# Optimization experiments

Measured on AMD Instinct MI355X. Metric: run time of the kernel, lower is better.

## Reference

```python
import jax, jax.numpy as jnp
import numpy as np

NUM_HEADS = 8
NUM_KV_HEADS = 2
HEAD_DIM = 64
EPS = 1e-6
ROPE_BASE = 10000.0


def rmsnorm(x, w):
    # x: (..., head_dim)
    var = jnp.mean(x * x, axis=-1, keepdims=True)
    return x * jax.lax.rsqrt(var + EPS) * w


def apply_rope(x):
    # x: (B, L, nH, hd); positions along L, standard rotate-half RoPE
    B, L, nH, hd = x.shape
    inv_freq = 1.0 / (ROPE_BASE ** (jnp.arange(0, hd, 2, dtype=jnp.float32) / hd))  # (hd/2,)
    ang = jnp.arange(L, dtype=jnp.float32)[:, None] * inv_freq[None, :]  # (L, hd/2)
    cos = jnp.concatenate([jnp.cos(ang), jnp.cos(ang)], axis=-1)[None, :, None, :]  # (1,L,1,hd)
    sin = jnp.concatenate([jnp.sin(ang), jnp.sin(ang)], axis=-1)[None, :, None, :]
    x1, x2 = jnp.split(x, 2, axis=-1)
    rot = jnp.concatenate([-x2, x1], axis=-1)
    return x * cos + rot * sin


def setup_inputs() -> dict:
    key = jax.random.key(0)
    ks = jax.random.split(key, 6)
    width = 512
    x = jax.random.normal(ks[0], (1, 16, 16, 16, width), dtype=jnp.float32)
    s = 1.0 / np.sqrt(width)
    Wq = jax.random.normal(ks[1], (width, width), dtype=jnp.float32) * s
    Wk = jax.random.normal(ks[2], (NUM_KV_HEADS * HEAD_DIM, width), dtype=jnp.float32) * s
    Wv = jax.random.normal(ks[3], (NUM_KV_HEADS * HEAD_DIM, width), dtype=jnp.float32) * s
    Wo = jax.random.normal(ks[4], (width, width), dtype=jnp.float32) * s
    q_norm_w = jnp.ones((HEAD_DIM,), dtype=jnp.float32)
    k_norm_w = jnp.ones((HEAD_DIM,), dtype=jnp.float32)
    return {"x": x, "Wq": Wq, "Wk": Wk, "Wv": Wv,
            "q_norm_w": q_norm_w, "k_norm_w": k_norm_w, "Wo": Wo}


def reference(x, Wq, Wk, Wv, q_norm_w, k_norm_w, Wo):
    B, H, W, D, C = x.shape
    L = H * W * D
    xf = x.reshape(B, L, C)
    q = (xf @ Wq.T).reshape(B, L, NUM_HEADS, HEAD_DIM)
    k = (xf @ Wk.T).reshape(B, L, NUM_KV_HEADS, HEAD_DIM)
    v = (xf @ Wv.T).reshape(B, L, NUM_KV_HEADS, HEAD_DIM)
    q = apply_rope(rmsnorm(q, q_norm_w))
    k = apply_rope(rmsnorm(k, k_norm_w))
    # (B, heads, L, hd)
    q = q.transpose(0, 2, 1, 3)
    k = k.transpose(0, 2, 1, 3)
    v = v.transpose(0, 2, 1, 3)
    repeats = NUM_HEADS // NUM_KV_HEADS
    if repeats > 1:
        k = jnp.repeat(k, repeats, axis=1)
        v = jnp.repeat(v, repeats, axis=1)
    scale = 1.0 / np.sqrt(HEAD_DIM)
    scores = jnp.einsum('bhqd,bhkd->bhqk', q, k) * scale
    attn = jax.nn.softmax(scores, axis=-1)
    out = jnp.einsum('bhqk,bhkd->bhqd', attn, v)
    out = out.transpose(0, 2, 1, 3).reshape(B, H, W, D, C)
    return out @ Wo.T
```

## Files before the change

### kernel.cpp

```cpp
#include <hip/hip_runtime.h>
#include <hip/hip_bf16.h>
#include <math.h>

#define L_SEQ 4096
#define CDIM  512
#define NH    8
#define NKV   2
#define HD    64
#define EPS   1e-6f
#define QSCALE 0.18033688011f

using short8 = __attribute__((ext_vector_type(8))) short;
using f32x4  = __attribute__((ext_vector_type(4))) float;
using f32x16 = __attribute__((ext_vector_type(16))) float;
typedef unsigned short ushort_t;

__device__ __forceinline__ ushort_t f2bf(float f) {
    union { float f; unsigned u; } c; c.f = f;
    unsigned r = c.u + 0x7FFF + ((c.u >> 16) & 1);
    return (ushort_t)(r >> 16);
}
__device__ __forceinline__ float bf2f(ushort_t u) {
    union { unsigned u; float f; } c; c.u = ((unsigned)u) << 16;
    return c.f;
}

#define GLOAD_LDS16(g, l)                                                  \
    __builtin_amdgcn_global_load_lds(                                      \
        (const __attribute__((address_space(1))) unsigned int*)(g),        \
        (__attribute__((address_space(3))) unsigned int*)(l), 16, 0, 0)

__device__ __forceinline__ short8 lds_read8(const char* p) {
    return *reinterpret_cast<const short8*>(__builtin_assume_aligned(p, 16));
}

__device__ __forceinline__ unsigned pk_bf16(float lo, float hi) {
    const __hip_bfloat162 h2 = __float22bfloat162_rn(make_float2(lo, hi));
    unsigned w; __builtin_memcpy(&w, &h2, 4);
    return w;
}

__global__ __launch_bounds__(256) void cvt_bf16(const float* __restrict__ x,
                                                const float* __restrict__ wq,
                                                const float* __restrict__ wk,
                                                const float* __restrict__ wv,
                                                const float* __restrict__ wo,
                                                ushort_t* __restrict__ xb,
                                                ushort_t* __restrict__ wqb,
                                                ushort_t* __restrict__ wkb,
                                                ushort_t* __restrict__ wvb,
                                                ushort_t* __restrict__ wob) {
    const size_t i = ((size_t)blockIdx.x * 256 + threadIdx.x) << 2;
    const float* s; ushort_t* d; size_t o;
    if (i < 2097152)      { s = x;  d = xb;  o = i; }
    else if (i < 2359296) { s = wq; d = wqb; o = i - 2097152; }
    else if (i < 2424832) { s = wk; d = wkb; o = i - 2359296; }
    else if (i < 2490368) { s = wv; d = wvb; o = i - 2424832; }
    else                  { s = wo; d = wob; o = i - 2490368; }
    const float4 v = *reinterpret_cast<const float4*>(s + o);
    ushort_t r[4] = { f2bf(v.x), f2bf(v.y), f2bf(v.z), f2bf(v.w) };
    *reinterpret_cast<uint2*>(d + o) = *reinterpret_cast<const uint2*>(r);
}

template<bool OUT_BF16>
__global__ __launch_bounds__(256) void gemm_bf16_nt(const ushort_t* __restrict__ A,
                                                    const ushort_t* __restrict__ B,
                                                    void* __restrict__ Cv,
                                                    int M, int N, int K) {
    __shared__ short As[2][4096];
    __shared__ short Bs[2][4096];

    const int tid = threadIdx.x;
    const int w = tid >> 6, lane = tid & 63;
    const int g = lane >> 4, r16 = lane & 15;
    const int wr = w >> 1, wc = w & 1;
    const int m0 = blockIdx.y * 64, n0 = blockIdx.x * 64;
    const int r7sw = (r16 & 7) << 4;

    const int lrow = lane >> 3;
    const int swzb = ((lane & 7) ^ lrow) << 4;
    const int c0 = w * 2, c1 = w * 2 + 1;
    const size_t rowK2 = (size_t)K * 2;

    const char* agA = (const char*)A + (size_t)(m0 + c0 * 8 + lrow) * rowK2 + swzb;
    const char* agB = agA + 8 * rowK2;
    const char* bgA = (const char*)B + (size_t)(n0 + c0 * 8 + lrow) * rowK2 + swzb;
    const char* bgB = bgA + 8 * rowK2;

    GLOAD_LDS16(agA, (char*)As[0] + c0 * 1024);
    GLOAD_LDS16(agB, (char*)As[0] + c1 * 1024);
    GLOAD_LDS16(bgA, (char*)Bs[0] + c0 * 1024);
    GLOAD_LDS16(bgB, (char*)Bs[0] + c1 * 1024);
    __syncthreads();

    f32x4 acc[2][2] = {};
    const int NKIT = K >> 6;
    int cur = 0;
    for (int it = 0; it < NKIT; ++it) {
        if (it + 1 < NKIT) {
            const size_t ko = (size_t)(it + 1) * 128;
            char* ad = (char*)As[cur ^ 1];
            char* bd = (char*)Bs[cur ^ 1];
            GLOAD_LDS16(agA + ko, ad + c0 * 1024);
            GLOAD_LDS16(agB + ko, ad + c1 * 1024);
            GLOAD_LDS16(bgA + ko, bd + c0 * 1024);
            GLOAD_LDS16(bgB + ko, bd + c1 * 1024);
        }
        const char* at = (const char*)As[cur];
        const char* bt = (const char*)Bs[cur];

        short8 af[2][2], bfr[2][2];
#pragma unroll
        for (int t = 0; t < 2; ++t)
#pragma unroll
            for (int ks = 0; ks < 2; ++ks) {
                af[t][ks]  = lds_read8(at + (wr * 32 + t * 16 + r16) * 128
                                          + ((ks * 64 + g * 16) ^ r7sw));
                bfr[t][ks] = lds_read8(bt + (wc * 32 + t * 16 + r16) * 128
                                          + ((ks * 64 + g * 16) ^ r7sw));
            }
        __builtin_amdgcn_s_setprio(1);
#pragma unroll
        for (int tm = 0; tm < 2; ++tm)
#pragma unroll
            for (int tn = 0; tn < 2; ++tn)
#pragma unroll
                for (int ks = 0; ks < 2; ++ks)
                    acc[tm][tn] = __builtin_amdgcn_mfma_f32_16x16x32_bf16(
                        af[tm][ks], bfr[tn][ks], acc[tm][tn], 0, 0, 0);
        __builtin_amdgcn_s_setprio(0);

        __syncthreads();
        cur ^= 1;
    }

#pragma unroll
    for (int tm = 0; tm < 2; ++tm)
#pragma unroll
        for (int tn = 0; tn < 2; ++tn)
#pragma unroll
            for (int jj = 0; jj < 4; ++jj) {
                const int row = m0 + wr * 32 + tm * 16 + g * 4 + jj;
                const int col = n0 + wc * 32 + tn * 16 + r16;
                if (OUT_BF16)
                    ((ushort_t*)Cv)[(size_t)row * N + col] = f2bf(acc[tm][tn][jj]);
                else
                    ((float*)Cv)[(size_t)row * N + col] = acc[tm][tn][jj];
            }
}

__global__ __launch_bounds__(256) void norm_rope(ushort_t* __restrict__ q,
                                                 ushort_t* __restrict__ k,
                                                 const float* __restrict__ qw,
                                                 const float* __restrict__ kw) {
    const int wid  = threadIdx.x >> 6;
    const int lane = threadIdx.x & 63;
    const long row = (long)blockIdx.x * 4 + wid;
    const long QROWS = (long)L_SEQ * NH;

    ushort_t* ptr;
    const float* w;
    int pos;
    const bool isq = (row < QROWS);
    if (isq) {
        pos = (int)(row >> 3);
        ptr = q + (size_t)pos * (NH * HD) + (int)(row & 7) * HD;
        w = qw;
    } else {
        const long r = row - QROWS;
        pos = (int)(r >> 1);
        ptr = k + (size_t)pos * (NKV * HD) + (int)(r & 1) * HD;
        w = kw;
    }

    float x = bf2f(ptr[lane]);
    float ss = x * x;
#pragma unroll
    for (int off = 32; off; off >>= 1) ss += __shfl_xor(ss, off);
    float xn = x * rsqrtf(ss * (1.0f / 64.0f) + EPS) * w[lane];

    float xp = __shfl_xor(xn, 32);
    const int i = lane & 31;
    const float inv_freq = exp2f((float)i * -0.41524101186f);
    float s, c;
    sincosf((float)pos * inv_freq, &s, &c);
    float out = (lane < 32) ? (xn * c - xp * s) : (xn * c + xp * s);
    if (isq) out *= QSCALE;
    ptr[lane] = f2bf(out);
}

__global__ __launch_bounds__(256, 4) void attn_mfma(const ushort_t* __restrict__ qb,
                                                    const ushort_t* __restrict__ kb,
                                                    const ushort_t* __restrict__ vtb,
                                                    ushort_t* __restrict__ opart,
                                                    float* __restrict__ lpart) {
    __shared__ short Ks[2][4096];
    __shared__ short Vs[2][4096];

    const int tid = threadIdx.x;
    const int w = tid >> 6, lane = tid & 63;
    const int l31 = lane & 31, hf = lane >> 5;
    const int h = blockIdx.y, hkv = h >> 2;
    const int s = blockIdx.z;
    const int kvspan = L_SEQ / gridDim.z;
    const int kvb = s * kvspan;
    const int qw = blockIdx.x * 128 + w * 32;
    const int swz = (lane & 7) << 4;

    const int lrow = lane >> 3;
    const int swzb = ((lane & 7) ^ lrow) << 4;
    const int c0 = w * 2, c1 = w * 2 + 1;

    const char* kgA = (const char*)kb + (size_t)(kvb + c0 * 8 + lrow) * (NKV * HD * 2)
                      + hkv * (HD * 2) + swzb;
    const char* kgB = kgA + 8 * (NKV * HD * 2);
    const char* vgA = (const char*)vtb + (size_t)(hkv * HD + c0 * 8 + lrow) * (L_SEQ * 2)
                      + (size_t)kvb * 2 + swzb;
    const char* vgB = vgA + 8 * (size_t)(L_SEQ * 2);

    short8 qf[4];
#pragma unroll
    for (int ks = 0; ks < 4; ++ks)
        qf[ks] = *reinterpret_cast<const short8*>(
            &qb[(size_t)(qw + l31) * CDIM + h * HD + ks * 16 + hf * 8]);

    short8 onesf;
    {
        const short ob = (l31 == 0) ? (short)0x3F80 : (short)0;
        onesf = short8{ob, ob, ob, ob, ob, ob, ob, ob};
    }

    GLOAD_LDS16(kgA, (char*)Ks[0] + c0 * 1024);
    GLOAD_LDS16(kgB, (char*)Ks[0] + c1 * 1024);
    GLOAD_LDS16(vgA, (char*)Vs[0] + c0 * 1024);
    GLOAD_LDS16(vgB, (char*)Vs[0] + c1 * 1024);
    __syncthreads();

    f32x16 oacc[2] = {};
    f32x16 oaccl = {};

    int cur = 0;
    const int nit = kvspan >> 6;
    for (int it = 0; it < nit; ++it) {
        if (it + 1 < nit) {
            const size_t ko = (size_t)(it + 1) * 64 * (NKV * HD * 2);
            const size_t vo = (size_t)(it + 1) * 128;
            char* kd = (char*)Ks[cur ^ 1];
            char* vd = (char*)Vs[cur ^ 1];
            GLOAD_LDS16(kgA + ko, kd + c0 * 1024);
            GLOAD_LDS16(kgB + ko, kd + c1 * 1024);
            GLOAD_LDS16(vgA + vo, vd + c0 * 1024);
            GLOAD_LDS16(vgB + vo, vd + c1 * 1024);
        }

        const char* kt = (const char*)Ks[cur];
        const char* vt = (const char*)Vs[cur];

        unsigned pkv[16];
#pragma unroll
        for (int sub = 0; sub < 2; ++sub) {
            f32x16 sacc = {};
            __builtin_amdgcn_s_setprio(1);
#pragma unroll
            for (int ks = 0; ks < 4; ++ks) {
                const short8 kf = lds_read8(
                    kt + (sub * 32 + l31) * 128 + ((ks * 32 + hf * 16) ^ swz));
                sacc = __builtin_amdgcn_mfma_f32_32x32x16_bf16(kf, qf[ks], sacc, 0, 0, 0);
            }
            __builtin_amdgcn_s_setprio(0);
#pragma unroll
            for (int r2 = 0; r2 < 8; ++r2)
                pkv[sub * 8 + r2] = pk_bf16(exp2f(sacc[2 * r2]), exp2f(sacc[2 * r2 + 1]));
        }

        short8 pfrag[4];
#pragma unroll
        for (int kk = 0; kk < 4; ++kk) {
            auto s0 = __builtin_amdgcn_permlane32_swap(pkv[kk * 4 + 0], pkv[kk * 4 + 2], false, false);
            auto s1 = __builtin_amdgcn_permlane32_swap(pkv[kk * 4 + 1], pkv[kk * 4 + 3], false, false);
            union { unsigned u[4]; short8 s8; } pf;
            pf.u[0] = s0[0]; pf.u[1] = s1[0]; pf.u[2] = s0[1]; pf.u[3] = s1[1];
            pfrag[kk] = pf.s8;
        }

        __builtin_amdgcn_s_setprio(1);
#pragma unroll
        for (int kk = 0; kk < 4; ++kk)
            oaccl = __builtin_amdgcn_mfma_f32_32x32x16_bf16(pfrag[kk], onesf, oaccl, 0, 0, 0);
#pragma unroll
        for (int n = 0; n < 2; ++n) {
#pragma unroll
            for (int kk = 0; kk < 4; ++kk) {
                const short8 vf = lds_read8(
                    vt + (n * 32 + l31) * 128 + ((kk * 32 + hf * 16) ^ swz));
                oacc[n] = __builtin_amdgcn_mfma_f32_32x32x16_bf16(pfrag[kk], vf, oacc[n], 0, 0, 0);
            }
        }
        __builtin_amdgcn_s_setprio(0);

        __syncthreads();
        cur ^= 1;
    }

    ushort_t* op = opart + (size_t)s * L_SEQ * CDIM;
#pragma unroll
    for (int n = 0; n < 2; ++n)
#pragma unroll
        for (int r = 0; r < 16; ++r) {
            const int row = qw + (r & 3) + 8 * (r >> 2) + 4 * hf;
            op[(size_t)row * CDIM + h * HD + n * 32 + l31] = f2bf(oacc[n][r]);
        }
    if (l31 == 0) {
        float* lp = lpart + (size_t)s * L_SEQ * NH;
#pragma unroll
        for (int r = 0; r < 16; ++r) {
            const int row = qw + (r & 3) + 8 * (r >> 2) + 4 * hf;
            lp[(size_t)row * NH + h] = oaccl[r];
        }
    }
}

__global__ __launch_bounds__(256) void combine_splits(const ushort_t* __restrict__ opart,
                                                      const float* __restrict__ lpart,
                                                      ushort_t* __restrict__ out,
                                                      int nsplit) {
    const size_t i4 = ((size_t)blockIdx.x * 256 + threadIdx.x) << 2;
    const int row = (int)(i4 >> 9);
    const int h = (int)((i4 & 511) >> 6);
    float l = 0.0f;
    for (int s = 0; s < nsplit; ++s)
        l += lpart[(size_t)s * L_SEQ * NH + (size_t)row * NH + h];
    const float inv = 1.0f / l;

    float acc[4] = {};
    for (int s = 0; s < nsplit; ++s) {
        ushort_t a[4];
        *reinterpret_cast<uint2*>(a) =
            *reinterpret_cast<const uint2*>(opart + (size_t)s * L_SEQ * CDIM + i4);
#pragma unroll
        for (int j = 0; j < 4; ++j) acc[j] += bf2f(a[j]);
    }
    ushort_t r[4];
#pragma unroll
    for (int j = 0; j < 4; ++j) r[j] = f2bf(acc[j] * inv);
    *reinterpret_cast<uint2*>(out + i4) = *reinterpret_cast<const uint2*>(r);
}

extern "C" void kernel_launch(void* const* d_in, const int* in_sizes, int n_in,
                              void* d_out, int out_size, void* d_ws, size_t ws_size,
                              hipStream_t stream) {
    const float* x   = (const float*)d_in[0];
    const float* Wq  = (const float*)d_in[1];
    const float* Wk  = (const float*)d_in[2];
    const float* Wv  = (const float*)d_in[3];
    const float* qnw = (const float*)d_in[4];
    const float* knw = (const float*)d_in[5];
    const float* Wo  = (const float*)d_in[6];
    float* out = (float*)d_out;

    const size_t tail = (size_t)L_SEQ * CDIM * 2
                      + (size_t)L_SEQ * NKV * HD * 2 * 2
                      + (size_t)CDIM * CDIM * 2 * 2
                      + (size_t)NKV * HD * CDIM * 2 * 2
                      + (size_t)8 * L_SEQ * NH * 4;
    const size_t need8 = (size_t)8 * L_SEQ * CDIM * 2 + tail;
    const int nsplit = (ws_size >= need8) ? 8 : 4;

    char* p = (char*)d_ws;
    ushort_t* opart = (ushort_t*)p;
    ushort_t* xb    = opart;
    ushort_t* abuf  = opart;
    char* q = p + (size_t)nsplit * L_SEQ * CDIM * 2;
    ushort_t* qbuf = (ushort_t*)q;
    ushort_t* kbuf = qbuf + (size_t)L_SEQ * CDIM;
    ushort_t* vtb  = kbuf + (size_t)L_SEQ * NKV * HD;
    ushort_t* wqb  = vtb  + (size_t)L_SEQ * NKV * HD;
    ushort_t* wkb  = wqb  + (size_t)CDIM * CDIM;
    ushort_t* wvb  = wkb  + (size_t)NKV * HD * CDIM;
    ushort_t* wob  = wvb  + (size_t)NKV * HD * CDIM;
    float*    lpart = (float*)(wob + (size_t)CDIM * CDIM);

    const dim3 blk(256);

    cvt_bf16<<<dim3(2688), blk, 0, stream>>>(x, Wq, Wk, Wv, Wo, xb, wqb, wkb, wvb, wob);

    gemm_bf16_nt<true><<<dim3(8, 64),  blk, 0, stream>>>(xb, wqb, qbuf, L_SEQ, CDIM, CDIM);
    gemm_bf16_nt<true><<<dim3(2, 64),  blk, 0, stream>>>(xb, wkb, kbuf, L_SEQ, NKV * HD, CDIM);
    gemm_bf16_nt<true><<<dim3(64, 2),  blk, 0, stream>>>(wvb, xb, vtb, NKV * HD, L_SEQ, CDIM);

    norm_rope<<<dim3((L_SEQ * (NH + NKV)) / 4), blk, 0, stream>>>(qbuf, kbuf, qnw, knw);

    attn_mfma<<<dim3(L_SEQ / 128, NH, nsplit), blk, 0, stream>>>(qbuf, kbuf, vtb, opart, lpart);

    combine_splits<<<dim3((L_SEQ * CDIM) / (256 * 4)), blk, 0, stream>>>(opart, lpart, abuf, nsplit);

    gemm_bf16_nt<false><<<dim3(8, 64), blk, 0, stream>>>(abuf, wob, out, L_SEQ, CDIM, CDIM);
}
```

Measured before the change: 112.3 us.

## Triple-buffer K/V loads with vmcnt waits and compute row sums in registers

Moves the attention kernel's K/V staging from double to triple buffering in LDS. It prefetches two tiles ahead and replaces the end-of-iteration __syncthreads with an explicit vmcnt wait plus barrier at the top of each iteration. It also drops the extra MFMA against a ones fragment that built the softmax denominators, accumulating the exp sums in scalar registers and reducing them across the half-wave at the end. Shared memory per block grows and the occupancy hint falls from 4 to 3 blocks. The denominator now sums the fp32 exps rather than their bf16-rounded values.

After: 111.4 us. No clear change (-0.8%).

```diff
diff --git a/kernel.cpp b/kernel.cpp
--- a/kernel.cpp
+++ b/kernel.cpp
@@ -189,13 +189,13 @@
     ptr[lane] = f2bf(out);
 }
 
-__global__ __launch_bounds__(256, 4) void attn_mfma(const ushort_t* __restrict__ qb,
+__global__ __launch_bounds__(256, 3) void attn_mfma(const ushort_t* __restrict__ qb,
                                                     const ushort_t* __restrict__ kb,
                                                     const ushort_t* __restrict__ vtb,
                                                     ushort_t* __restrict__ opart,
                                                     float* __restrict__ lpart) {
-    __shared__ short Ks[2][4096];
-    __shared__ short Vs[2][4096];
+    __shared__ short Ks[3][4096];
+    __shared__ short Vs[3][4096];
 
     const int tid = threadIdx.x;
     const int w = tid >> 6, lane = tid & 63;
@@ -224,37 +224,40 @@
         qf[ks] = *reinterpret_cast<const short8*>(
             &qb[(size_t)(qw + l31) * CDIM + h * HD + ks * 16 + hf * 8]);
 
-    short8 onesf;
     {
-        const short ob = (l31 == 0) ? (short)0x3F80 : (short)0;
-        onesf = short8{ob, ob, ob, ob, ob, ob, ob, ob};
-    }
-
-    GLOAD_LDS16(kgA, (char*)Ks[0] + c0 * 1024);
-    GLOAD_LDS16(kgB, (char*)Ks[0] + c1 * 1024);
-    GLOAD_LDS16(vgA, (char*)Vs[0] + c0 * 1024);
-    GLOAD_LDS16(vgB, (char*)Vs[0] + c1 * 1024);
-    __syncthreads();
+        GLOAD_LDS16(kgA, (char*)Ks[0] + c0 * 1024);
+        GLOAD_LDS16(kgB, (char*)Ks[0] + c1 * 1024);
+        GLOAD_LDS16(vgA, (char*)Vs[0] + c0 * 1024);
+        GLOAD_LDS16(vgB, (char*)Vs[0] + c1 * 1024);
+        const size_t ko = (size_t)64 * (NKV * HD * 2);
+        const size_t vo = 128;
+        GLOAD_LDS16(kgA + ko, (char*)Ks[1] + c0 * 1024);
+        GLOAD_LDS16(kgB + ko, (char*)Ks[1] + c1 * 1024);
+        GLOAD_LDS16(vgA + vo, (char*)Vs[1] + c0 * 1024);
+        GLOAD_LDS16(vgB + vo, (char*)Vs[1] + c1 * 1024);
+    }
 
     f32x16 oacc[2] = {};
-    f32x16 oaccl = {};
-
-    int cur = 0;
+    float lsum = 0.0f;
+
+    char* kc = (char*)Ks[0]; char* kn = (char*)Ks[1]; char* kf3 = (char*)Ks[2];
+    char* vc = (char*)Vs[0]; char* vn = (char*)Vs[1]; char* vf3 = (char*)Vs[2];
+
     const int nit = kvspan >> 6;
     for (int it = 0; it < nit; ++it) {
-        if (it + 1 < nit) {
-            const size_t ko = (size_t)(it + 1) * 64 * (NKV * HD * 2);
-            const size_t vo = (size_t)(it + 1) * 128;
-            char* kd = (char*)Ks[cur ^ 1];
-            char* vd = (char*)Vs[cur ^ 1];
-            GLOAD_LDS16(kgA + ko, kd + c0 * 1024);
-            GLOAD_LDS16(kgB + ko, kd + c1 * 1024);
-            GLOAD_LDS16(vgA + vo, vd + c0 * 1024);
-            GLOAD_LDS16(vgB + vo, vd + c1 * 1024);
-        }
-
-        const char* kt = (const char*)Ks[cur];
-        const char* vt = (const char*)Vs[cur];
+        if (it + 1 < nit) asm volatile("s_waitcnt vmcnt(4)" ::: "memory");
+        else              asm volatile("s_waitcnt vmcnt(0)" ::: "memory");
+        __builtin_amdgcn_s_barrier();
+        __builtin_amdgcn_sched_barrier(0);
+
+        if (it + 2 < nit) {
+            const size_t ko = (size_t)(it + 2) * 64 * (NKV * HD * 2);
+            const size_t vo = (size_t)(it + 2) * 128;
+            GLOAD_LDS16(kgA + ko, kf3 + c0 * 1024);
+            GLOAD_LDS16(kgB + ko, kf3 + c1 * 1024);
+            GLOAD_LDS16(vgA + vo, vf3 + c0 * 1024);
+            GLOAD_LDS16(vgB + vo, vf3 + c1 * 1024);
+        }
 
         unsigned pkv[16];
 #pragma unroll
@@ -263,14 +266,18 @@
             __builtin_amdgcn_s_setprio(1);
 #pragma unroll
             for (int ks = 0; ks < 4; ++ks) {
-                const short8 kf = lds_read8(
-                    kt + (sub * 32 + l31) * 128 + ((ks * 32 + hf * 16) ^ swz));
-                sacc = __builtin_amdgcn_mfma_f32_32x32x16_bf16(kf, qf[ks], sacc, 0, 0, 0);
+                const short8 kfr = lds_read8(
+                    kc + (sub * 32 + l31) * 128 + ((ks * 32 + hf * 16) ^ swz));
+                sacc = __builtin_amdgcn_mfma_f32_32x32x16_bf16(kfr, qf[ks], sacc, 0, 0, 0);
             }
             __builtin_amdgcn_s_setprio(0);
 #pragma unroll
-            for (int r2 = 0; r2 < 8; ++r2)
-                pkv[sub * 8 + r2] = pk_bf16(exp2f(sacc[2 * r2]), exp2f(sacc[2 * r2 + 1]));
+            for (int r2 = 0; r2 < 8; ++r2) {
+                const float x = exp2f(sacc[2 * r2]);
+                const float y = exp2f(sacc[2 * r2 + 1]);
+                lsum += x + y;
+                pkv[sub * 8 + r2] = pk_bf16(x, y);
+            }
         }
 
         short8 pfrag[4];
@@ -285,24 +292,24 @@
 
         __builtin_amdgcn_s_setprio(1);
 #pragma unroll
-        for (int kk = 0; kk < 4; ++kk)
-            oaccl = __builtin_amdgcn_mfma_f32_32x32x16_bf16(pfrag[kk], onesf, oaccl, 0, 0, 0);
-#pragma unroll
         for (int n = 0; n < 2; ++n) {
 #pragma unroll
             for (int kk = 0; kk < 4; ++kk) {
                 const short8 vf = lds_read8(
-                    vt + (n * 32 + l31) * 128 + ((kk * 32 + hf * 16) ^ swz));
+                    vc + (n * 32 + l31) * 128 + ((kk * 32 + hf * 16) ^ swz));
                 oacc[n] = __builtin_amdgcn_mfma_f32_32x32x16_bf16(pfrag[kk], vf, oacc[n], 0, 0, 0);
             }
         }
         __builtin_amdgcn_s_setprio(0);
 
-        __syncthreads();
-        cur ^= 1;
-    }
-
+        char* tk = kc; kc = kn; kn = kf3; kf3 = tk;
+        char* tv = vc; vc = vn; vn = vf3; vf3 = tv;
+    }
+
+    lsum += __shfl_xor(lsum, 32);
     ushort_t* op = opart + (size_t)s * L_SEQ * CDIM;
+    float* lp = lpart + (size_t)s * L_SEQ * NH;
+    if (lane < 32) lp[(size_t)(qw + lane) * NH + h] = lsum;
 #pragma unroll
     for (int n = 0; n < 2; ++n)
 #pragma unroll
@@ -310,14 +317,6 @@
             const int row = qw + (r & 3) + 8 * (r >> 2) + 4 * hf;
             op[(size_t)row * CDIM + h * HD + n * 32 + l31] = f2bf(oacc[n][r]);
         }
-    if (l31 == 0) {
-        float* lp = lpart + (size_t)s * L_SEQ * NH;
-#pragma unroll
-        for (int r = 0; r < 16; ++r) {
-            const int row = qw + (r & 3) + 8 * (r >> 2) + 4 * hf;
-            lp[(size_t)row * NH + h] = oaccl[r];
-        }
-    }
 }
 
 __global__ __launch_bounds__(256) void combine_splits(const ushort_t* __restrict__ opart,
```

## Double query rows per wave and compute softmax row sums with scalar adds

Applied to the files above, without the earlier changes.

Each wave now handles 64 query rows as two 32-row MFMA tiles. Every K and V fragment read from LDS is therefore reused twice, and the grid is halved. The row-sum computation moves from an extra ones-vector MFMA to per-lane float accumulation followed by a cross-half shuffle. PV accumulation is interleaved per sub-block to limit live registers. Register pressure roughly doubles, so the launch bound drops to 2 blocks per CU, which reduces occupancy and the number of blocks.

Result: slower. 115.1 us (+2.5%).

```diff
diff --git a/kernel.cpp b/kernel.cpp
--- a/kernel.cpp
+++ b/kernel.cpp
@@ -189,7 +189,7 @@
     ptr[lane] = f2bf(out);
 }
 
-__global__ __launch_bounds__(256, 4) void attn_mfma(const ushort_t* __restrict__ qb,
+__global__ __launch_bounds__(256, 2) void attn_mfma(const ushort_t* __restrict__ qb,
                                                     const ushort_t* __restrict__ kb,
                                                     const ushort_t* __restrict__ vtb,
                                                     ushort_t* __restrict__ opart,
@@ -204,7 +204,7 @@
     const int s = blockIdx.z;
     const int kvspan = L_SEQ / gridDim.z;
     const int kvb = s * kvspan;
-    const int qw = blockIdx.x * 128 + w * 32;
+    const int qw = blockIdx.x * 256 + w * 64;
     const int swz = (lane & 7) << 4;
 
     const int lrow = lane >> 3;
@@ -218,16 +218,13 @@
                       + (size_t)kvb * 2 + swzb;
     const char* vgB = vgA + 8 * (size_t)(L_SEQ * 2);
 
-    short8 qf[4];
-#pragma unroll
-    for (int ks = 0; ks < 4; ++ks)
-        qf[ks] = *reinterpret_cast<const short8*>(
+    short8 qf0[4], qf1[4];
+#pragma unroll
+    for (int ks = 0; ks < 4; ++ks) {
+        qf0[ks] = *reinterpret_cast<const short8*>(
             &qb[(size_t)(qw + l31) * CDIM + h * HD + ks * 16 + hf * 8]);
-
-    short8 onesf;
-    {
-        const short ob = (l31 == 0) ? (short)0x3F80 : (short)0;
-        onesf = short8{ob, ob, ob, ob, ob, ob, ob, ob};
+        qf1[ks] = *reinterpret_cast<const short8*>(
+            &qb[(size_t)(qw + 32 + l31) * CDIM + h * HD + ks * 16 + hf * 8]);
     }
 
     GLOAD_LDS16(kgA, (char*)Ks[0] + c0 * 1024);
@@ -236,8 +233,8 @@
     GLOAD_LDS16(vgB, (char*)Vs[0] + c1 * 1024);
     __syncthreads();
 
-    f32x16 oacc[2] = {};
-    f32x16 oaccl = {};
+    f32x16 oacc0[2] = {}, oacc1[2] = {};
+    float ls0[2] = {}, ls1[2] = {};
 
     int cur = 0;
     const int nit = kvspan >> 6;
@@ -256,68 +253,79 @@
         const char* kt = (const char*)Ks[cur];
         const char* vt = (const char*)Vs[cur];
 
-        unsigned pkv[16];
 #pragma unroll
         for (int sub = 0; sub < 2; ++sub) {
-            f32x16 sacc = {};
+            f32x16 s0 = {}, s1 = {};
             __builtin_amdgcn_s_setprio(1);
 #pragma unroll
             for (int ks = 0; ks < 4; ++ks) {
-                const short8 kf = lds_read8(
+                const short8 kfr = lds_read8(
                     kt + (sub * 32 + l31) * 128 + ((ks * 32 + hf * 16) ^ swz));
-                sacc = __builtin_amdgcn_mfma_f32_32x32x16_bf16(kf, qf[ks], sacc, 0, 0, 0);
+                s0 = __builtin_amdgcn_mfma_f32_32x32x16_bf16(kfr, qf0[ks], s0, 0, 0, 0);
+                s1 = __builtin_amdgcn_mfma_f32_32x32x16_bf16(kfr, qf1[ks], s1, 0, 0, 0);
             }
             __builtin_amdgcn_s_setprio(0);
-#pragma unroll
-            for (int r2 = 0; r2 < 8; ++r2)
-                pkv[sub * 8 + r2] = pk_bf16(exp2f(sacc[2 * r2]), exp2f(sacc[2 * r2 + 1]));
+
+            unsigned pk0[8], pk1[8];
+#pragma unroll
+            for (int r2 = 0; r2 < 8; ++r2) {
+                const float x0 = exp2f(s0[2 * r2]), y0 = exp2f(s0[2 * r2 + 1]);
+                const float x1 = exp2f(s1[2 * r2]), y1 = exp2f(s1[2 * r2 + 1]);
+                ls0[r2 & 1] += x0 + y0;
+                ls1[r2 & 1] += x1 + y1;
+                pk0[r2] = pk_bf16(x0, y0);
+                pk1[r2] = pk_bf16(x1, y1);
+            }
+
+            short8 pf0[2], pf1[2];
+#pragma unroll
+            for (int kkl = 0; kkl < 2; ++kkl) {
+                auto a0 = __builtin_amdgcn_permlane32_swap(pk0[kkl * 4 + 0], pk0[kkl * 4 + 2], false, false);
+                auto a1 = __builtin_amdgcn_permlane32_swap(pk0[kkl * 4 + 1], pk0[kkl * 4 + 3], false, false);
+                auto b0 = __builtin_amdgcn_permlane32_swap(pk1[kkl * 4 + 0], pk1[kkl * 4 + 2], false, false);
+                auto b1 = __builtin_amdgcn_permlane32_swap(pk1[kkl * 4 + 1], pk1[kkl * 4 + 3], false, false);
+                union { unsigned u[4]; short8 s8; } u0, u1;
+                u0.u[0] = a0[0]; u0.u[1] = a1[0]; u0.u[2] = a0[1]; u0.u[3] = a1[1];
+                u1.u[0] = b0[0]; u1.u[1] = b1[0]; u1.u[2] = b0[1]; u1.u[3] = b1[1];
+                pf0[kkl] = u0.s8; pf1[kkl] = u1.s8;
+            }
+
+            __builtin_amdgcn_s_setprio(1);
+#pragma unroll
+            for (int n = 0; n < 2; ++n) {
+#pragma unroll
+                for (int kkl = 0; kkl < 2; ++kkl) {
+                    const short8 vf = lds_read8(
+                        vt + (n * 32 + l31) * 128 + (((sub * 2 + kkl) * 32 + hf * 16) ^ swz));
+                    oacc0[n] = __builtin_amdgcn_mfma_f32_32x32x16_bf16(pf0[kkl], vf, oacc0[n], 0, 0, 0);
+                    oacc1[n] = __builtin_amdgcn_mfma_f32_32x32x16_bf16(pf1[kkl], vf, oacc1[n], 0, 0, 0);
+                }
+            }
+            __builtin_amdgcn_s_setprio(0);
         }
-
-        short8 pfrag[4];
-#pragma unroll
-        for (int kk = 0; kk < 4; ++kk) {
-            auto s0 = __builtin_amdgcn_permlane32_swap(pkv[kk * 4 + 0], pkv[kk * 4 + 2], false, false);
-            auto s1 = __builtin_amdgcn_permlane32_swap(pkv[kk * 4 + 1], pkv[kk * 4 + 3], false, false);
-            union { unsigned u[4]; short8 s8; } pf;
-            pf.u[0] = s0[0]; pf.u[1] = s1[0]; pf.u[2] = s0[1]; pf.u[3] = s1[1];
-            pfrag[kk] = pf.s8;
-        }
-
-        __builtin_amdgcn_s_setprio(1);
-#pragma unroll
-        for (int kk = 0; kk < 4; ++kk)
-            oaccl = __builtin_amdgcn_mfma_f32_32x32x16_bf16(pfrag[kk], onesf, oaccl, 0, 0, 0);
-#pragma unroll
-        for (int n = 0; n < 2; ++n) {
-#pragma unroll
-            for (int kk = 0; kk < 4; ++kk) {
-                const short8 vf = lds_read8(
-                    vt + (n * 32 + l31) * 128 + ((kk * 32 + hf * 16) ^ swz));
-                oacc[n] = __builtin_amdgcn_mfma_f32_32x32x16_bf16(pfrag[kk], vf, oacc[n], 0, 0, 0);
-            }
-        }
-        __builtin_amdgcn_s_setprio(0);
 
         __syncthreads();
         cur ^= 1;
     }
 
+    float lsA = ls0[0] + ls0[1];
+    float lsB = ls1[0] + ls1[1];
+    lsA += __shfl_xor(lsA, 32);
+    lsB += __shfl_xor(lsB, 32);
     ushort_t* op = opart + (size_t)s * L_SEQ * CDIM;
+    float* lp = lpart + (size_t)s * L_SEQ * NH;
+    if (lane < 32) {
+        lp[(size_t)(qw + lane) * NH + h] = lsA;
+        lp[(size_t)(qw + 32 + lane) * NH + h] = lsB;
+    }
 #pragma unroll
     for (int n = 0; n < 2; ++n)
 #pragma unroll
         for (int r = 0; r < 16; ++r) {
-            const int row = qw + (r & 3) + 8 * (r >> 2) + 4 * hf;
-            op[(size_t)row * CDIM + h * HD + n * 32 + l31] = f2bf(oacc[n][r]);
+            const int rr = (r & 3) + 8 * (r >> 2) + 4 * hf;
+            op[(size_t)(qw + rr) * CDIM + h * HD + n * 32 + l31] = f2bf(oacc0[n][r]);
+            op[(size_t)(qw + 32 + rr) * CDIM + h * HD + n * 32 + l31] = f2bf(oacc1[n][r]);
         }
-    if (l31 == 0) {
-        float* lp = lpart + (size_t)s * L_SEQ * NH;
-#pragma unroll
-        for (int r = 0; r < 16; ++r) {
-            const int row = qw + (r & 3) + 8 * (r >> 2) + 4 * hf;
-            lp[(size_t)row * NH + h] = oaccl[r];
-        }
-    }
 }
 
 __global__ __launch_bounds__(256) void combine_splits(const ushort_t* __restrict__ opart,
@@ -390,7 +398,7 @@
 
     norm_rope<<<dim3((L_SEQ * (NH + NKV)) / 4), blk, 0, stream>>>(qbuf, kbuf, qnw, knw);
 
-    attn_mfma<<<dim3(L_SEQ / 128, NH, nsplit), blk, 0, stream>>>(qbuf, kbuf, vtb, opart, lpart);
+    attn_mfma<<<dim3(L_SEQ / 256, NH, nsplit), blk, 0, stream>>>(qbuf, kbuf, vtb, opart, lpart);
 
     combine_splits<<<dim3((L_SEQ * CDIM) / (256 * 4)), blk, 0, stream>>>(opart, lpart, abuf, nsplit);
 
```
